# Performance work log

Measured on AMD Instinct MI355X. Metric: run time of the kernel, lower is better.

Reference implementation:

```python
import jax, jax.numpy as jnp
import numpy as np

T, B, I, H = 512, 64, 256, 512


def setup_inputs() -> dict:
    key = jax.random.key(0)
    ks = jax.random.split(key, 17)
    s_in = 1.0 / np.sqrt(I)  # nn.Linear default init bound
    s_h = 1.0 / np.sqrt(H)

    def u(k, shape, s):
        return jax.random.uniform(k, shape, jnp.float32, -s, s)

    inp = {"x": jax.random.normal(ks[0], (T, B, I), jnp.float32)}
    idx = 1
    for n in ["f", "i", "o", "c"]:
        inp[f"W{n}"] = u(ks[idx], (H, I), s_in); idx += 1
        inp[f"bW{n}"] = u(ks[idx], (H,), s_in); idx += 1
    for n in ["f", "i", "o", "c"]:
        inp[f"U{n}"] = u(ks[idx], (H, H), s_h); idx += 1
        inp[f"bU{n}"] = u(ks[idx], (H,), s_h); idx += 1
    return inp


def reference(x, Wf, bWf, Wi, bWi, Wo, bWo, Wc, bWc,
              Uf, bUf, Ui, bUi, Uo, bUo, Uc, bUc):
    Hd = Wf.shape[0]
    # Fuse the 4 input-projection GEMMs into one big (T*B, I) x (I, 4H) GEMM,
    # folding both bias sets in (same math as Wg(x_t)+Ug(h) per gate).
    Wall = jnp.concatenate([Wf, Wi, Wo, Wc], axis=0)          # (4H, I)
    Uall = jnp.concatenate([Uf, Ui, Uo, Uc], axis=0)          # (4H, H)
    ball = jnp.concatenate([bWf + bUf, bWi + bUi, bWo + bUo, bWc + bUc], axis=0)
    xW = jnp.einsum('tbi,gi->tbg', x, Wall) + ball            # (T, B, 4H)

    def step(carry, xw_t):
        h, c = carry                                          # (B, H) each
        g = xw_t + h @ Uall.T                                 # (B, 4H)
        f = jax.nn.sigmoid(g[:, :Hd])
        i = jax.nn.sigmoid(g[:, Hd:2 * Hd])
        o = jax.nn.sigmoid(g[:, 2 * Hd:3 * Hd])
        c = f * c + i * jnp.tanh(g[:, 3 * Hd:])
        h = o * jnp.tanh(c)
        return (h, c), h

    Bsz = x.shape[1]
    h0 = jnp.zeros((Bsz, Hd), x.dtype)
    c0 = jnp.zeros((Bsz, Hd), x.dtype)
    (h, c), h_seq = jax.lax.scan(step, (h0, c0), xW)
    # torch code cats (1,B,H) tensors along 0 -> (T,B,H); final states keep (1,B,H)
    return h_seq, h[None], c[None]
```

## Files before the change

### kernel.cpp

```cpp
#include <hip/hip_runtime.h>
#include <cstdint>
#include <cstddef>


typedef __attribute__((ext_vector_type(8))) short short8;
typedef __attribute__((ext_vector_type(4))) float float4v;

__device__ __forceinline__ unsigned short f2bf(float f) {
  unsigned u = __float_as_uint(f);
  u = u + 0x7FFFu + ((u >> 16) & 1u);
  return (unsigned short)(u >> 16);
}
__device__ __forceinline__ float bf2f(unsigned short s) {
  return __uint_as_float(((unsigned)s) << 16);
}
__device__ __forceinline__ unsigned long long pack4(float4 v) {
  return (unsigned long long)f2bf(v.x) |
         ((unsigned long long)f2bf(v.y) << 16) |
         ((unsigned long long)f2bf(v.z) << 32) |
         ((unsigned long long)f2bf(v.w) << 48);
}

__global__ void prep_kernel(
    const float* __restrict__ Wf, const float* __restrict__ bWf,
    const float* __restrict__ Wi, const float* __restrict__ bWi,
    const float* __restrict__ Wo, const float* __restrict__ bWo,
    const float* __restrict__ Wc, const float* __restrict__ bWc,
    const float* __restrict__ Uf, const float* __restrict__ bUf,
    const float* __restrict__ Ui, const float* __restrict__ bUi,
    const float* __restrict__ Uo, const float* __restrict__ bUo,
    const float* __restrict__ Uc, const float* __restrict__ bUc,
    unsigned short* __restrict__ Wall, unsigned short* __restrict__ Uall,
    float* __restrict__ ball, int* __restrict__ flags)
{
  const float* Ws[4]  = {Wf, Wi, Wo, Wc};
  const float* Us[4]  = {Uf, Ui, Uo, Uc};
  const float* bWs[4] = {bWf, bWi, bWo, bWc};
  const float* bUs[4] = {bUf, bUi, bUo, bUc};
  const long long NW4 = 131072;
  const long long NU4 = 262144;
  const long long NB4 = 512;
  const long long TOT = NW4 + NU4 + NB4;
  long long idx0 = (long long)blockIdx.x * blockDim.x + threadIdx.x;
  if (idx0 < 64) flags[idx0] = 0;
  long long stride = (long long)gridDim.x * blockDim.x;
  for (long long u = idx0; u < TOT; u += stride) {
    if (u < NW4) {
      int e = (int)(u << 2);
      int n = e >> 8, k = e & 255;
      float4 v = *(const float4*)(Ws[n >> 9] + (size_t)(n & 511) * 256 + k);
      ((unsigned long long*)Wall)[u] = pack4(v);
    } else if (u < NW4 + NU4) {
      long long q = u - NW4;
      int e = (int)(q << 2);
      int n = e >> 9, k = e & 511;
      float4 v = *(const float4*)(Us[n >> 9] + (size_t)(n & 511) * 512 + k);
      ((unsigned long long*)Uall)[q] = pack4(v);
    } else {
      long long q = u - NW4 - NU4;
      int e = (int)(q << 2);
      int gate = e >> 9, r = e & 511;
      float4 a = *(const float4*)(bWs[gate] + r);
      float4 b = *(const float4*)(bUs[gate] + r);
      float4 sv;
      sv.x = a.x + b.x; sv.y = a.y + b.y; sv.z = a.z + b.z; sv.w = a.w + b.w;
      *(float4*)(ball + e) = sv;
    }
  }
}

__global__ __launch_bounds__(256, 2) void xw_gemm(
    const float* __restrict__ x,
    const unsigned short* __restrict__ Wall,
    const float* __restrict__ ball,
    unsigned short* __restrict__ xw)
{
  __shared__ short As[128 * 72];
  __shared__ short Bs[128 * 72];
  const int tid = threadIdx.x;
  const int bn = blockIdx.x, bm = blockIdx.y;
  const int Mbase = bm * 128, Nbase = bn * 128;
  const int w = tid >> 6, L = tid & 63, lq = L >> 4, lr = L & 15;
  const int wm = w >> 1, wn = w & 1;
  const int srow = tid >> 1, shalf = tid & 1;

  float4v acc[4][4];
  #pragma unroll
  for (int a = 0; a < 4; ++a)
    #pragma unroll
    for (int b = 0; b < 4; ++b) acc[a][b] = (float4v){0.f, 0.f, 0.f, 0.f};

  for (int ko = 0; ko < 256; ko += 64) {
    const float* gaf = x + (size_t)(Mbase + srow) * 256 + ko + shalf * 32;
    float4 f0 = *(const float4*)(gaf);
    float4 f1 = *(const float4*)(gaf + 4);
    float4 f2 = *(const float4*)(gaf + 8);
    float4 f3 = *(const float4*)(gaf + 12);
    float4 f4 = *(const float4*)(gaf + 16);
    float4 f5 = *(const float4*)(gaf + 20);
    float4 f6 = *(const float4*)(gaf + 24);
    float4 f7 = *(const float4*)(gaf + 28);
    const unsigned short* gb = Wall + (size_t)(Nbase + srow) * 256 + ko + shalf * 32;
    short8 b0 = *(const short8*)(gb);
    short8 b1 = *(const short8*)(gb + 8);
    short8 b2 = *(const short8*)(gb + 16);
    short8 b3 = *(const short8*)(gb + 24);
    __syncthreads();
    {
      unsigned long long* pa = (unsigned long long*)&As[srow * 72 + shalf * 32];
      pa[0] = pack4(f0); pa[1] = pack4(f1);
      pa[2] = pack4(f2); pa[3] = pack4(f3);
      pa[4] = pack4(f4); pa[5] = pack4(f5);
      pa[6] = pack4(f6); pa[7] = pack4(f7);
      short* pb = &Bs[srow * 72 + shalf * 32];
      *(short8*)(pb) = b0; *(short8*)(pb + 8) = b1;
      *(short8*)(pb + 16) = b2; *(short8*)(pb + 24) = b3;
    }
    __syncthreads();
    #pragma unroll
    for (int kk = 0; kk < 64; kk += 32) {
      short8 af[4], bfr[4];
      #pragma unroll
      for (int mi = 0; mi < 4; ++mi)
        af[mi] = *(const short8*)&As[(wm * 64 + mi * 16 + lr) * 72 + kk + lq * 8];
      #pragma unroll
      for (int ni = 0; ni < 4; ++ni)
        bfr[ni] = *(const short8*)&Bs[(wn * 64 + ni * 16 + lr) * 72 + kk + lq * 8];
      #pragma unroll
      for (int mi = 0; mi < 4; ++mi)
        #pragma unroll
        for (int ni = 0; ni < 4; ++ni)
          acc[mi][ni] = __builtin_amdgcn_mfma_f32_16x16x32_bf16(
              af[mi], bfr[ni], acc[mi][ni], 0, 0, 0);
    }
  }
  #pragma unroll
  for (int ni = 0; ni < 4; ++ni) {
    int col = Nbase + wn * 64 + ni * 16 + lr;
    float bias = ball[col];
    #pragma unroll
    for (int mi = 0; mi < 4; ++mi) {
      #pragma unroll
      for (int r = 0; r < 4; ++r) {
        int row = Mbase + wm * 64 + mi * 16 + lq * 4 + r;
        xw[(size_t)row * 2048 + col] = f2bf(acc[mi][ni][r] + bias);
      }
    }
  }
}

__global__ __launch_bounds__(256, 1) void lstm_scan(
    const unsigned short* __restrict__ xw,
    const unsigned short* __restrict__ Uall,
    unsigned short* __restrict__ hbuf,
    int* __restrict__ flags,
    float* __restrict__ out)
{
  __shared__ short hstage[16 * 520];
  __shared__ float gates[4 * 16 * 33];
  __shared__ unsigned short xwb[4 * 16 * 32];

  const int tid = threadIdx.x;
  const int wg = blockIdx.x;
  const int g = wg >> 4;
  const int s = wg & 15;
  const int w = tid >> 6, L = tid & 63, lq = L >> 4, lr = L & 15;

  const int eb = tid >> 4;
  const int ej = (tid & 15) * 2;
  const int xb = tid >> 4, xg = (tid >> 2) & 3, xc = tid & 3;

  float* hseq = out;
  float* hfin = out + (size_t)512 * 64 * 512;
  float* cfin = hfin + (size_t)64 * 512;
  int* grp_flags = flags + g * 16;

  short8 uf[2][16];
  #pragma unroll
  for (int nt = 0; nt < 2; ++nt)
    #pragma unroll
    for (int kt = 0; kt < 16; ++kt) {
      const unsigned short* p = Uall +
          (size_t)(w * 512 + s * 32 + nt * 16 + lr) * 512 + kt * 32 + lq * 8;
      uf[nt][kt] = *(const short8*)p;
    }

  float c0 = 0.f, c1 = 0.f, h0 = 0.f, h1 = 0.f;

  for (int t = 0; t < 512; ++t) {
    const unsigned short* xp = xw +
        ((size_t)(t * 64 + g * 16 + xb)) * 2048 + xg * 512 + s * 32 + xc * 8;
    short8 xv = *(const short8*)xp;

    float4v a0a = (float4v){0.f, 0.f, 0.f, 0.f};
    float4v a0b = (float4v){0.f, 0.f, 0.f, 0.f};
    float4v a1a = (float4v){0.f, 0.f, 0.f, 0.f};
    float4v a1b = (float4v){0.f, 0.f, 0.f, 0.f};

    if (t > 0) {
      if (tid < 16) {
        while (__hip_atomic_load(&grp_flags[tid], __ATOMIC_RELAXED,
                                 __HIP_MEMORY_SCOPE_AGENT) < t)
          __builtin_amdgcn_s_sleep(1);
      }
      __syncthreads();
      const unsigned short* hsrc =
          hbuf + ((size_t)((t - 1) & 1)) * 32768 + (size_t)g * 8192;
      const int scol = (tid & 63) * 8;
      const int sr0 = tid >> 6;
      unsigned long long hv[8];
      #pragma unroll
      for (int r = 0; r < 4; ++r) {
        const unsigned long long* p = (const unsigned long long*)
            (hsrc + (size_t)(sr0 + r * 4) * 512 + scol);
        hv[2 * r]     = __hip_atomic_load(p, __ATOMIC_RELAXED,
                                          __HIP_MEMORY_SCOPE_AGENT);
        hv[2 * r + 1] = __hip_atomic_load(p + 1, __ATOMIC_RELAXED,
                                          __HIP_MEMORY_SCOPE_AGENT);
      }
      #pragma unroll
      for (int r = 0; r < 4; ++r) {
        unsigned long long* q =
            (unsigned long long*)&hstage[(sr0 + r * 4) * 520 + scol];
        q[0] = hv[2 * r]; q[1] = hv[2 * r + 1];
      }
      __syncthreads();
      #pragma unroll
      for (int kt = 0; kt < 8; ++kt) {
        short8 afA = *(const short8*)&hstage[lr * 520 + kt * 32 + lq * 8];
        short8 afB = *(const short8*)&hstage[lr * 520 + (kt + 8) * 32 + lq * 8];
        a0a = __builtin_amdgcn_mfma_f32_16x16x32_bf16(afA, uf[0][kt], a0a, 0, 0, 0);
        a0b = __builtin_amdgcn_mfma_f32_16x16x32_bf16(afB, uf[0][kt + 8], a0b, 0, 0, 0);
        a1a = __builtin_amdgcn_mfma_f32_16x16x32_bf16(afA, uf[1][kt], a1a, 0, 0, 0);
        a1b = __builtin_amdgcn_mfma_f32_16x16x32_bf16(afB, uf[1][kt + 8], a1b, 0, 0, 0);
      }
    }
    float4v acc0 = a0a + a0b;
    float4v acc1 = a1a + a1b;

    #pragma unroll
    for (int r = 0; r < 4; ++r) {
      gates[w * 528 + (lq * 4 + r) * 33 + lr] = acc0[r];
      gates[w * 528 + (lq * 4 + r) * 33 + 16 + lr] = acc1[r];
    }
    *(short8*)&xwb[xg * 512 + xb * 32 + xc * 8] = xv;
    __syncthreads();

    {
      float gf = gates[eb * 33 + ej] + bf2f(xwb[eb * 32 + ej]);
      float gi = gates[528 + eb * 33 + ej] + bf2f(xwb[512 + eb * 32 + ej]);
      float go = gates[1056 + eb * 33 + ej] + bf2f(xwb[1024 + eb * 32 + ej]);
      float gc = gates[1584 + eb * 33 + ej] + bf2f(xwb[1536 + eb * 32 + ej]);
      float f_ = 1.f / (1.f + __expf(-gf));
      float i_ = 1.f / (1.f + __expf(-gi));
      float o_ = 1.f / (1.f + __expf(-go));
      float ct = 1.f - 2.f / (__expf(2.f * gc) + 1.f);
      c0 = f_ * c0 + i_ * ct;
      h0 = o_ * (1.f - 2.f / (__expf(2.f * c0) + 1.f));
    }
    {
      int j = ej + 1;
      float gf = gates[eb * 33 + j] + bf2f(xwb[eb * 32 + j]);
      float gi = gates[528 + eb * 33 + j] + bf2f(xwb[512 + eb * 32 + j]);
      float go = gates[1056 + eb * 33 + j] + bf2f(xwb[1024 + eb * 32 + j]);
      float gc = gates[1584 + eb * 33 + j] + bf2f(xwb[1536 + eb * 32 + j]);
      float f_ = 1.f / (1.f + __expf(-gf));
      float i_ = 1.f / (1.f + __expf(-gi));
      float o_ = 1.f / (1.f + __expf(-go));
      float ct = 1.f - 2.f / (__expf(2.f * gc) + 1.f);
      c1 = f_ * c1 + i_ * ct;
      h1 = o_ * (1.f - 2.f / (__expf(2.f * c1) + 1.f));
    }
    size_t orow = ((size_t)(t * 64 + g * 16 + eb)) * 512 + s * 32 + ej;
    {
      float2 hv2 = make_float2(h0, h1);
      __builtin_nontemporal_store(*(double*)&hv2, (double*)(hseq + orow));
    }
    unsigned hb = ((unsigned)f2bf(h1) << 16) | (unsigned)f2bf(h0);
    unsigned* hdst = (unsigned*)(hbuf + ((size_t)(t & 1)) * 32768 +
                                 ((size_t)(g * 16 + eb)) * 512 + s * 32 + ej);
    __hip_atomic_store(hdst, hb, __ATOMIC_RELAXED, __HIP_MEMORY_SCOPE_AGENT);

    __syncthreads();
    if (tid == 0)
      __hip_atomic_store(&grp_flags[s], t + 1, __ATOMIC_RELAXED,
                         __HIP_MEMORY_SCOPE_AGENT);
  }

  size_t fo = ((size_t)(g * 16 + eb)) * 512 + s * 32 + ej;
  *(float2*)(hfin + fo) = make_float2(h0, h1);
  *(float2*)(cfin + fo) = make_float2(c0, c1);
}

extern "C" void kernel_launch(void* const* d_in, const int* in_sizes, int n_in,
                              void* d_out, int out_size, void* d_ws, size_t ws_size,
                              hipStream_t stream) {
  (void)in_sizes; (void)n_in; (void)out_size; (void)ws_size;
  const float* x   = (const float*)d_in[0];
  const float* Wf  = (const float*)d_in[1];
  const float* bWf = (const float*)d_in[2];
  const float* Wi  = (const float*)d_in[3];
  const float* bWi = (const float*)d_in[4];
  const float* Wo  = (const float*)d_in[5];
  const float* bWo = (const float*)d_in[6];
  const float* Wc  = (const float*)d_in[7];
  const float* bWc = (const float*)d_in[8];
  const float* Uf  = (const float*)d_in[9];
  const float* bUf = (const float*)d_in[10];
  const float* Ui  = (const float*)d_in[11];
  const float* bUi = (const float*)d_in[12];
  const float* Uo  = (const float*)d_in[13];
  const float* bUo = (const float*)d_in[14];
  const float* Uc  = (const float*)d_in[15];
  const float* bUc = (const float*)d_in[16];

  char* ws = (char*)d_ws;
  unsigned short* xw   = (unsigned short*)(ws);
  unsigned short* Wall = (unsigned short*)(ws + 134217728);
  unsigned short* Uall = (unsigned short*)(ws + 135266304);
  float*          ball = (float*)         (ws + 137363456);
  unsigned short* hbuf = (unsigned short*)(ws + 137371648);
  int*            flags= (int*)           (ws + 137502720);

  prep_kernel<<<768, 256, 0, stream>>>(Wf, bWf, Wi, bWi, Wo, bWo, Wc, bWc,
                                       Uf, bUf, Ui, bUi, Uo, bUo, Uc, bUc,
                                       Wall, Uall, ball, flags);
  xw_gemm<<<dim3(16, 256), 256, 0, stream>>>(x, Wall, ball, xw);
  lstm_scan<<<64, 256, 0, stream>>>(xw, Uall, hbuf, flags, (float*)d_out);
}
```

Measured before the change: 1.544 ms.

## Replace per-step flag barrier with step-tagged hidden-state words for inter-block sync

Each hidden-state pair is now written as a 64-bit word that carries the timestep in its upper half. Consumers spin directly on the data words until every tag matches the previous step, instead of polling per-workgroup flags. This removes the end-of-step __syncthreads, the separate flag store and the flag-wait-then-load round trip, so cross-block latency on the serial recurrence is lower. In exchange the hidden-state buffer doubles in size, and every thread spins on 16 global atomic loads, which can add memory traffic while waiting.

New measurement: 1.673 ms. +8.4%, slower.

```diff
diff --git a/kernel.cpp b/kernel.cpp
--- a/kernel.cpp
+++ b/kernel.cpp
@@ -31,7 +31,7 @@
     const float* __restrict__ Uo, const float* __restrict__ bUo,
     const float* __restrict__ Uc, const float* __restrict__ bUc,
     unsigned short* __restrict__ Wall, unsigned short* __restrict__ Uall,
-    float* __restrict__ ball, int* __restrict__ flags)
+    float* __restrict__ ball, unsigned long long* __restrict__ hbuf)
 {
   const float* Ws[4]  = {Wf, Wi, Wo, Wc};
   const float* Us[4]  = {Uf, Ui, Uo, Uc};
@@ -42,7 +42,7 @@
   const long long NB4 = 512;
   const long long TOT = NW4 + NU4 + NB4;
   long long idx0 = (long long)blockIdx.x * blockDim.x + threadIdx.x;
-  if (idx0 < 64) flags[idx0] = 0;
+  if (idx0 < 32768) hbuf[idx0] = 0xFFFFFFFF00000000ULL;
   long long stride = (long long)gridDim.x * blockDim.x;
   for (long long u = idx0; u < TOT; u += stride) {
     if (u < NW4) {
@@ -152,8 +152,7 @@
 __global__ __launch_bounds__(256, 1) void lstm_scan(
     const unsigned short* __restrict__ xw,
     const unsigned short* __restrict__ Uall,
-    unsigned short* __restrict__ hbuf,
-    int* __restrict__ flags,
+    unsigned long long* __restrict__ hbuf,
     float* __restrict__ out)
 {
   __shared__ short hstage[16 * 520];
@@ -173,7 +172,6 @@
   float* hseq = out;
   float* hfin = out + (size_t)512 * 64 * 512;
   float* cfin = hfin + (size_t)64 * 512;
-  int* grp_flags = flags + g * 16;
 
   short8 uf[2][16];
   #pragma unroll
@@ -198,32 +196,30 @@
     float4v a1b = (float4v){0.f, 0.f, 0.f, 0.f};
 
     if (t > 0) {
-      if (tid < 16) {
-        while (__hip_atomic_load(&grp_flags[tid], __ATOMIC_RELAXED,
-                                 __HIP_MEMORY_SCOPE_AGENT) < t)
-          __builtin_amdgcn_s_sleep(1);
+      unsigned long long* hb =
+          hbuf + ((size_t)((t - 1) & 1)) * 16384 + (size_t)g * 4096;
+      const unsigned want = (unsigned)(t - 1);
+      unsigned long long hv[16];
+      bool ok[16];
+      #pragma unroll
+      for (int k = 0; k < 16; ++k) ok[k] = false;
+      for (;;) {
+        #pragma unroll
+        for (int k = 0; k < 16; ++k)
+          if (!ok[k])
+            hv[k] = __hip_atomic_load(&hb[k * 256 + tid], __ATOMIC_RELAXED,
+                                      __HIP_MEMORY_SCOPE_AGENT);
+        bool all = true;
+        #pragma unroll
+        for (int k = 0; k < 16; ++k) {
+          ok[k] = ok[k] || ((unsigned)(hv[k] >> 32) == want);
+          all = all && ok[k];
+        }
+        if (all) break;
       }
-      __syncthreads();
-      const unsigned short* hsrc =
-          hbuf + ((size_t)((t - 1) & 1)) * 32768 + (size_t)g * 8192;
-      const int scol = (tid & 63) * 8;
-      const int sr0 = tid >> 6;
-      unsigned long long hv[8];
-      #pragma unroll
-      for (int r = 0; r < 4; ++r) {
-        const unsigned long long* p = (const unsigned long long*)
-            (hsrc + (size_t)(sr0 + r * 4) * 512 + scol);
-        hv[2 * r]     = __hip_atomic_load(p, __ATOMIC_RELAXED,
-                                          __HIP_MEMORY_SCOPE_AGENT);
-        hv[2 * r + 1] = __hip_atomic_load(p + 1, __ATOMIC_RELAXED,
-                                          __HIP_MEMORY_SCOPE_AGENT);
-      }
-      #pragma unroll
-      for (int r = 0; r < 4; ++r) {
-        unsigned long long* q =
-            (unsigned long long*)&hstage[(sr0 + r * 4) * 520 + scol];
-        q[0] = hv[2 * r]; q[1] = hv[2 * r + 1];
-      }
+      #pragma unroll
+      for (int k = 0; k < 16; ++k)
+        *(unsigned*)&hstage[k * 520 + tid * 2] = (unsigned)hv[k];
       __syncthreads();
       #pragma unroll
       for (int kt = 0; kt < 8; ++kt) {
@@ -271,20 +267,20 @@
       c1 = f_ * c1 + i_ * ct;
       h1 = o_ * (1.f - 2.f / (__expf(2.f * c1) + 1.f));
     }
+
+    unsigned payload = ((unsigned)f2bf(h1) << 16) | (unsigned)f2bf(h0);
+    unsigned long long word =
+        (((unsigned long long)(unsigned)t) << 32) | (unsigned long long)payload;
+    __hip_atomic_store(
+        hbuf + ((size_t)(t & 1)) * 16384 + ((size_t)(g * 16 + eb)) * 256 +
+            (size_t)(s * 16 + (tid & 15)),
+        word, __ATOMIC_RELAXED, __HIP_MEMORY_SCOPE_AGENT);
+
     size_t orow = ((size_t)(t * 64 + g * 16 + eb)) * 512 + s * 32 + ej;
     {
       float2 hv2 = make_float2(h0, h1);
       __builtin_nontemporal_store(*(double*)&hv2, (double*)(hseq + orow));
     }
-    unsigned hb = ((unsigned)f2bf(h1) << 16) | (unsigned)f2bf(h0);
-    unsigned* hdst = (unsigned*)(hbuf + ((size_t)(t & 1)) * 32768 +
-                                 ((size_t)(g * 16 + eb)) * 512 + s * 32 + ej);
-    __hip_atomic_store(hdst, hb, __ATOMIC_RELAXED, __HIP_MEMORY_SCOPE_AGENT);
-
-    __syncthreads();
-    if (tid == 0)
-      __hip_atomic_store(&grp_flags[s], t + 1, __ATOMIC_RELAXED,
-                         __HIP_MEMORY_SCOPE_AGENT);
   }
 
   size_t fo = ((size_t)(g * 16 + eb)) * 512 + s * 32 + ej;
@@ -319,12 +315,12 @@
   unsigned short* Wall = (unsigned short*)(ws + 134217728);
   unsigned short* Uall = (unsigned short*)(ws + 135266304);
   float*          ball = (float*)         (ws + 137363456);
-  unsigned short* hbuf = (unsigned short*)(ws + 137371648);
-  int*            flags= (int*)           (ws + 137502720);
+  unsigned long long* hbuf =
+      (unsigned long long*)(ws + 137371648);
 
   prep_kernel<<<768, 256, 0, stream>>>(Wf, bWf, Wi, bWi, Wo, bWo, Wc, bWc,
                                        Uf, bUf, Ui, bUi, Uo, bUo, Uc, bUc,
-                                       Wall, Uall, ball, flags);
+                                       Wall, Uall, ball, hbuf);
   xw_gemm<<<dim3(16, 256), 256, 0, stream>>>(x, Wall, ball, xw);
-  lstm_scan<<<64, 256, 0, stream>>>(xw, Uall, hbuf, flags, (float*)d_out);
-}
+  lstm_scan<<<64, 256, 0, stream>>>(xw, Uall, hbuf, (float*)d_out);
+}
```
